# Kernel optimization log

Hardware: AMD Instinct MI355X
Metric: run time of the kernel (lower is better)

The kernel has to match this reference:

```python
import jax, jax.numpy as jnp
import numpy as np

N, IN_RAW, H, E, UNROLLS = 1024, 10, 96, 16384, 2

def _p(key, shape):
    return jax.random.normal(key, shape, dtype=jnp.float32) * 0.05

def setup_inputs() -> dict:
    key = jax.random.key(0)
    ks = jax.random.split(key, 24)
    x = jax.random.normal(ks[0], (N, IN_RAW), dtype=jnp.float32)
    edge_index = jax.random.randint(ks[1], (2, E), 0, N, dtype=jnp.int64)
    adj = jax.random.randint(ks[2], (N, N), 0, 2, dtype=jnp.int32)
    return {
        'x': x, 'edge_index': edge_index, 'adj': adj,
        # init_layer
        'W_init': _p(ks[3], (H, IN_RAW - 1)), 'b_init': _p(ks[4], (H,)),
        # GatedGraphConv (num_layers=1): weight [H,H], GRUCell params
        'W_ggc': _p(ks[5], (H, H)),
        'W_ih': _p(ks[6], (3 * H, H)), 'W_hh': _p(ks[7], (3 * H, H)),
        'b_ih': _p(ks[8], (3 * H,)), 'b_hh': _p(ks[9], (3 * H,)),
        # edge_attention: Linear(2H->H), Linear(H->1)
        'Wa1': _p(ks[10], (H, 2 * H)), 'ba1': _p(ks[11], (H,)),
        'Wa2': _p(ks[12], (1, H)), 'ba2': _p(ks[13], (1,)),
        # out MLP
        'Wo1': _p(ks[14], (H, H)), 'bo1': _p(ks[15], (H,)),
        'Wo2': _p(ks[16], (H, H)), 'bo2': _p(ks[17], (H,)),
        # heads
        'Wp1': _p(ks[18], (1, H)), 'bp1': _p(ks[19], (1,)),
        'Wp2': _p(ks[20], (1, H)), 'bp2': _p(ks[21], (1,)),
    }

def _leaky(v):
    return jnp.where(v >= 0, v, 0.01 * v)  # LeakyReLU default slope

def _ggnn_forward(x, edge_index, adj,
                  W_init, b_init, W_ggc, W_ih, W_hh, b_ih, b_hh,
                  Wa1, ba1, Wa2, ba2, Wo1, bo1, Wo2, bo2,
                  Wp1, bp1, Wp2, bp2):
    src, tgt = edge_index[0], edge_index[1]
    x = x[:, :-1]                                   # data.x[:, :-1]
    x = _leaky(x @ W_init.T + b_init)               # [N,H]
    adj_mask = (adj == 1)
    for _ in range(UNROLLS):
        # GatedGraphConv, 1 layer, aggr='mean'
        m = x @ W_ggc                               # [N,H]
        s = jax.ops.segment_sum(m[src], tgt, num_segments=N)
        cnt = jax.ops.segment_sum(jnp.ones((E,), x.dtype), tgt, num_segments=N)
        agg = s / jnp.maximum(cnt, 1.0)[:, None]    # mean, 0 for isolated nodes
        # GRUCell(agg, x)
        gi = agg @ W_ih.T + b_ih
        gh = x @ W_hh.T + b_hh
        ir, iz, inn = jnp.split(gi, 3, axis=1)
        hr, hz, hn = jnp.split(gh, 3, axis=1)
        r = jax.nn.sigmoid(ir + hr)
        z = jax.nn.sigmoid(iz + hz)
        n = jnp.tanh(inn + r * hn)
        x = (1.0 - z) * n + z * x
        # edge attention: concat(x_i, x_j) -> Linear(2H->H) decomposed into
        # two [H,H] halves so the NxNx2H concat tensor is never materialized.
        hi = x @ Wa1[:, :H].T                       # acts on t1 (row i)
        hj = x @ Wa1[:, H:].T                       # acts on t2 (row j)
        h = jax.nn.sigmoid(hi[:, None, :] + hj[None, :, :] + ba1)  # [N,N,H]
        coeffs = jax.nn.sigmoid(h @ Wa2[0] + ba2[0])               # [N,N]
        coeffs = jnp.where(adj_mask, coeffs, 0.0)
        x = coeffs @ x
    x = _leaky(x @ Wo1.T + bo1)
    x = _leaky(x @ Wo2.T + bo2)
    out1 = jax.nn.sigmoid(x @ Wp1.T + bp1)
    out2 = jax.nn.sigmoid(x @ Wp2.T + bp2)
    return out1, out2

def reference(x, edge_index, adj,
              W_init, b_init, W_ggc, W_ih, W_hh, b_ih, b_hh,
              Wa1, ba1, Wa2, ba2, Wo1, bo1, Wo2, bo2,
              Wp1, bp1, Wp2, bp2):
    return _ggnn_forward(x, edge_index, adj,
                         W_init, b_init, W_ggc, W_ih, W_hh, b_ih, b_hh,
                         Wa1, ba1, Wa2, ba2, Wo1, bo1, Wo2, bo2,
                         Wp1, bp1, Wp2, bp2)
```

## Files before the change

### kernel.cpp

```cpp
#include <hip/hip_runtime.h>

#define Nn 1024
#define Hh 96
#define Ee 16384
#define IN_K 9
#define IN_STRIDE 10
#define NH (Nn * Hh)
#define XS 128
#define SLOTS 64

__device__ __forceinline__ float sigf(float v) {
    return __builtin_amdgcn_rcpf(1.0f + __expf(-v));
}
__device__ __forceinline__ float tanhfast(float v) {
    float e = __expf(2.0f * v);
    return (e - 1.0f) * __builtin_amdgcn_rcpf(e + 1.0f);
}
__device__ __forceinline__ float leakyf(float v) {
    return v >= 0.0f ? v : 0.01f * v;
}

__global__ __launch_bounds__(256) void setup_kernel(
    const float* __restrict__ W_hh, const float* __restrict__ Wa1,
    const float* __restrict__ Wo1, const float* __restrict__ Wo2,
    const float* __restrict__ W_ggc, const float* __restrict__ W_ih,
    const float* __restrict__ x_in, const float* __restrict__ W_init,
    const float* __restrict__ b_init,
    float* __restrict__ Wt_hh, float* __restrict__ Wt_a1i,
    float* __restrict__ Wt_a1j, float* __restrict__ Wt_o1,
    float* __restrict__ Wt_o2, float* __restrict__ Wf,
    int* __restrict__ deg, float* __restrict__ xA)
{
    int gt = blockIdx.x * 256 + threadIdx.x;
    if (gt < Nn) deg[gt] = 0;
    if (gt < 64512) {
        int idx = gt;
        if (idx < 27648) {
            int k = idx / 288, c = idx % 288;
            Wt_hh[idx] = W_hh[c * 96 + k];
        } else if ((idx -= 27648) < 9216) {
            int k = idx / 96, h = idx % 96;
            Wt_a1i[idx] = Wa1[h * 192 + k];
        } else if ((idx -= 9216) < 9216) {
            int k = idx / 96, h = idx % 96;
            Wt_a1j[idx] = Wa1[h * 192 + 96 + k];
        } else if ((idx -= 9216) < 9216) {
            int k = idx / 96, j = idx % 96;
            Wt_o1[idx] = Wo1[j * 96 + k];
        } else {
            idx -= 9216;
            int k = idx / 96, j = idx % 96;
            Wt_o2[idx] = Wo2[j * 96 + k];
        }
    }
    if (gt < 27648) {
        int k = gt / 288, c = gt % 288;
        const float* g = W_ggc + k * 96;
        const float* w = W_ih + c * 96;
        float acc = 0.0f;
        for (int j = 0; j < 96; ++j) acc += g[j] * w[j];
        Wf[gt] = acc;
    }
    if (gt < NH) {
        int n = gt / Hh, j = gt - n * Hh;
        const float* xr = x_in + n * IN_STRIDE;
        const float* wr = W_init + j * IN_K;
        float acc = b_init[j];
#pragma unroll
        for (int k = 0; k < IN_K; ++k) acc += xr[k] * wr[k];
        xA[n * XS + j] = leakyf(acc);
    }
}

__global__ __launch_bounds__(256) void edges_kernel(
    const int* __restrict__ ei, int* __restrict__ deg, int* __restrict__ bucket)
{
    int e = blockIdx.x * 256 + threadIdx.x;
    if (e >= Ee) return;
    int src = ei[e];
    int tgt = ei[Ee + e];
    int slot = atomicAdd(&deg[tgt], 1);
    if (slot < SLOTS) bucket[tgt * SLOTS + slot] = src;
}

__global__ __launch_bounds__(384) void gru_kernel(
    const float* __restrict__ xA, const int* __restrict__ deg,
    const int* __restrict__ bucket,
    const float* __restrict__ Wf, const float* __restrict__ Wt_hh,
    const float* __restrict__ b_ih, const float* __restrict__ b_hh,
    const float* __restrict__ Wt_a1i, const float* __restrict__ Wt_a1j,
    const float* __restrict__ ba1,
    float* __restrict__ xB, float* __restrict__ Ei, float* __restrict__ EjT)
{
    __shared__ float Pp[2][2][Hh];
    __shared__ float Pm[2][Hh];
    __shared__ float Xr[2][Hh];
    __shared__ float Xo[2][Hh];
    __shared__ float red6[2][2][Hh][6];
    __shared__ float redp[2][2][Hh][2];
    int tid = threadIdx.x;
    int half = tid / 192;
    int loc = tid - half * 192;
    int r = loc / Hh, h = loc - r * Hh;
    int n = blockIdx.x * 2 + r;
    {
        int d = deg[n];
        int dc = d < SLOTS ? d : SLOTS;
        const int* bk = bucket + n * SLOTS;
        float acc = 0.0f;
        for (int s = half; s < dc; s += 2)
            acc += xA[bk[s] * XS + h];
        Pp[half][r][h] = acc;
        if (half == 0) Xr[r][h] = xA[n * XS + h];
    }
    __syncthreads();
    if (half == 0) {
        float inv = __builtin_amdgcn_rcpf(fmaxf((float)deg[n], 1.0f));
        Pm[r][h] = (Pp[0][r][h] + Pp[1][r][h]) * inv;
    }
    __syncthreads();
    {
        const float* Pr = Pm[r];
        const float* xr = Xr[r];
        const float* pf = Wf + h;
        const float* ph = Wt_hh + h;
        float gir = 0.f, giz = 0.f, gin = 0.f;
        float ghr = 0.f, ghz = 0.f, ghn = 0.f;
        int k0 = half * 48;
#pragma unroll 4
        for (int k = k0; k < k0 + 48; ++k) {
            float a = Pr[k];
            float xv = xr[k];
            int o = k * 288;
            gir += a * pf[o];
            giz += a * pf[o + 96];
            gin += a * pf[o + 192];
            ghr += xv * ph[o];
            ghz += xv * ph[o + 96];
            ghn += xv * ph[o + 192];
        }
        red6[half][r][h][0] = gir;
        red6[half][r][h][1] = giz;
        red6[half][r][h][2] = gin;
        red6[half][r][h][3] = ghr;
        red6[half][r][h][4] = ghz;
        red6[half][r][h][5] = ghn;
    }
    __syncthreads();
    if (half == 0) {
        float gir = b_ih[h] + red6[0][r][h][0] + red6[1][r][h][0];
        float giz = b_ih[Hh + h] + red6[0][r][h][1] + red6[1][r][h][1];
        float gin = b_ih[2 * Hh + h] + red6[0][r][h][2] + red6[1][r][h][2];
        float ghr = b_hh[h] + red6[0][r][h][3] + red6[1][r][h][3];
        float ghz = b_hh[Hh + h] + red6[0][r][h][4] + red6[1][r][h][4];
        float ghn = b_hh[2 * Hh + h] + red6[0][r][h][5] + red6[1][r][h][5];
        float rr = sigf(gir + ghr);
        float z = sigf(giz + ghz);
        float nn2 = tanhfast(gin + rr * ghn);
        float xo = (1.0f - z) * nn2 + z * Xr[r][h];
        xB[n * XS + h] = xo;
        Xo[r][h] = xo;
    }
    __syncthreads();
    {
        const float* row = Xo[r];
        const float* wi = Wt_a1i + h;
        const float* wj = Wt_a1j + h;
        float a = 0.0f, bb = 0.0f;
        int k0 = half * 48;
#pragma unroll 4
        for (int k = k0; k < k0 + 48; ++k) {
            float xv = row[k];
            a += xv * wi[k * 96];
            bb += xv * wj[k * 96];
        }
        redp[half][r][h][0] = a;
        redp[half][r][h][1] = bb;
    }
    __syncthreads();
    if (half == 0) {
        float a = redp[0][r][h][0] + redp[1][r][h][0];
        float bb = redp[0][r][h][1] + redp[1][r][h][1];
        Ei[n * Hh + h] = __expf(-(a + ba1[h]));
        EjT[h * Nn + n] = __expf(-bb);
    }
}

template <bool HEAD>
__global__ __launch_bounds__(512) void attn_kernel(
    const float* __restrict__ Ei, const float* __restrict__ EjT,
    const float* __restrict__ Wa2, const float* __restrict__ ba2,
    const int* __restrict__ adj, const float* __restrict__ xB,
    float* __restrict__ xA,
    const float* __restrict__ Wt_o1, const float* __restrict__ bo1,
    const float* __restrict__ Wt_o2, const float* __restrict__ bo2,
    const float* __restrict__ Wp1, const float* __restrict__ bp1,
    const float* __restrict__ Wp2, const float* __restrict__ bp2,
    float* __restrict__ out)
{
    __shared__ __align__(16) float wa2[Hh];
    __shared__ __align__(16) float eis[2][Hh];
    __shared__ __align__(16) float C[2][Nn];
    __shared__ float red[4][2][Hh];
    __shared__ float xout[2][Hh];
    __shared__ float t1[2][Hh];
    __shared__ float t2[2][Hh];
    int tid = threadIdx.x;
    int i0 = blockIdx.x * 2;
    if (tid < Hh) wa2[tid] = Wa2[tid];
    if (tid < 2 * Hh) {
        int r = tid / Hh, h = tid - r * Hh;
        eis[r][h] = Ei[(i0 + r) * Hh + h];
    }
    __syncthreads();
    {
        int row = tid >> 8;
        int jj = (tid & 255) * 4;
        int4 mk = *(const int4*)(adj + (i0 + row) * Nn + jj);
        float s0 = 0.f, s1 = 0.f, s2 = 0.f, s3 = 0.f;
        const float* er = eis[row];
#pragma unroll 4
        for (int k = 0; k < Hh; ++k) {
            float4 e4 = *(const float4*)(EjT + k * Nn + jj);
            float eik = er[k];
            float wk = wa2[k];
            s0 += __builtin_amdgcn_rcpf(fmaf(eik, e4.x, 1.0f)) * wk;
            s1 += __builtin_amdgcn_rcpf(fmaf(eik, e4.y, 1.0f)) * wk;
            s2 += __builtin_amdgcn_rcpf(fmaf(eik, e4.z, 1.0f)) * wk;
            s3 += __builtin_amdgcn_rcpf(fmaf(eik, e4.w, 1.0f)) * wk;
        }
        float b2 = ba2[0];
        float4 c;
        c.x = (mk.x == 1) ? sigf(s0 + b2) : 0.0f;
        c.y = (mk.y == 1) ? sigf(s1 + b2) : 0.0f;
        c.z = (mk.z == 1) ? sigf(s2 + b2) : 0.0f;
        c.w = (mk.w == 1) ? sigf(s3 + b2) : 0.0f;
        *(float4*)(&C[row][jj]) = c;
    }
    __syncthreads();
    {
        int q = tid >> 7;
        int h = tid & 127;
        if (h < Hh) {
            const float* xc = xB + h;
            int jb = q * 256;
            const float* c0 = &C[0][jb];
            const float* c1 = &C[1][jb];
            float acc0 = 0.f, acc1 = 0.f;
#pragma unroll 4
            for (int j = 0; j < 256; ++j) {
                float xv = xc[(jb + j) * XS];
                acc0 += c0[j] * xv;
                acc1 += c1[j] * xv;
            }
            red[q][0][h] = acc0;
            red[q][1][h] = acc1;
        }
        __syncthreads();
        if (q == 0 && h < Hh) {
#pragma unroll
            for (int r = 0; r < 2; ++r) {
                float v = red[0][r][h] + red[1][r][h] + red[2][r][h] + red[3][r][h];
                if (HEAD) xout[r][h] = v;
                else      xA[(i0 + r) * XS + h] = v;
            }
        }
    }
    if (HEAD) {
        __syncthreads();
        if (tid < 2 * Hh) {
            int r = tid / Hh, h = tid - r * Hh;
            const float* w = Wt_o1 + h;
            float acc = bo1[h];
            for (int k = 0; k < Hh; ++k) acc += xout[r][k] * w[k * 96];
            t1[r][h] = leakyf(acc);
        }
        __syncthreads();
        if (tid < 2 * Hh) {
            int r = tid / Hh, h = tid - r * Hh;
            const float* w = Wt_o2 + h;
            float acc = bo2[h];
            for (int k = 0; k < Hh; ++k) acc += t1[r][k] * w[k * 96];
            t2[r][h] = leakyf(acc);
        }
        __syncthreads();
        if (tid < 4) {
            int r = tid >> 1, which = tid & 1;
            const float* wp = which ? Wp2 : Wp1;
            float acc = 0.f;
            for (int k = 0; k < Hh; ++k) acc += t2[r][k] * wp[k];
            float b = which ? bp2[0] : bp1[0];
            out[which * Nn + i0 + r] = sigf(acc + b);
        }
    }
}

extern "C" void kernel_launch(void* const* d_in, const int* in_sizes, int n_in,
                              void* d_out, int out_size, void* d_ws, size_t ws_size,
                              hipStream_t stream)
{
    const float* x_in   = (const float*)d_in[0];
    const int*   ei     = (const int*)d_in[1];
    const int*   adj    = (const int*)d_in[2];
    const float* W_init = (const float*)d_in[3];
    const float* b_init = (const float*)d_in[4];
    const float* W_ggc  = (const float*)d_in[5];
    const float* W_ih   = (const float*)d_in[6];
    const float* W_hh   = (const float*)d_in[7];
    const float* b_ih   = (const float*)d_in[8];
    const float* b_hh   = (const float*)d_in[9];
    const float* Wa1    = (const float*)d_in[10];
    const float* ba1    = (const float*)d_in[11];
    const float* Wa2    = (const float*)d_in[12];
    const float* ba2    = (const float*)d_in[13];
    const float* Wo1    = (const float*)d_in[14];
    const float* bo1    = (const float*)d_in[15];
    const float* Wo2    = (const float*)d_in[16];
    const float* bo2    = (const float*)d_in[17];
    const float* Wp1    = (const float*)d_in[18];
    const float* bp1    = (const float*)d_in[19];
    const float* Wp2    = (const float*)d_in[20];
    const float* bp2    = (const float*)d_in[21];
    float* out = (float*)d_out;

    float* ws     = (float*)d_ws;
    float* xA     = ws;
    float* xB     = xA + Nn * XS;
    float* Ei     = xB + Nn * XS;
    float* EjT    = Ei + NH;
    float* Wt_hh  = EjT + NH;
    float* Wf     = Wt_hh + 27648;
    float* Wt_a1i = Wf + 27648;
    float* Wt_a1j = Wt_a1i + 9216;
    float* Wt_o1  = Wt_a1j + 9216;
    float* Wt_o2  = Wt_o1 + 9216;
    int*   deg    = (int*)(Wt_o2 + 9216);
    int*   bucket = deg + Nn;

    setup_kernel<<<(NH + 255) / 256, 256, 0, stream>>>(
        W_hh, Wa1, Wo1, Wo2, W_ggc, W_ih, x_in, W_init, b_init,
        Wt_hh, Wt_a1i, Wt_a1j, Wt_o1, Wt_o2, Wf, deg, xA);
    edges_kernel<<<(Ee + 255) / 256, 256, 0, stream>>>(ei, deg, bucket);

    gru_kernel<<<Nn / 2, 384, 0, stream>>>(
        xA, deg, bucket, Wf, Wt_hh, b_ih, b_hh, Wt_a1i, Wt_a1j, ba1,
        xB, Ei, EjT);
    attn_kernel<false><<<Nn / 2, 512, 0, stream>>>(
        Ei, EjT, Wa2, ba2, adj, xB, xA,
        nullptr, nullptr, nullptr, nullptr, nullptr, nullptr, nullptr, nullptr,
        nullptr);
    gru_kernel<<<Nn / 2, 384, 0, stream>>>(
        xA, deg, bucket, Wf, Wt_hh, b_ih, b_hh, Wt_a1i, Wt_a1j, ba1,
        xB, Ei, EjT);
    attn_kernel<true><<<Nn / 2, 512, 0, stream>>>(
        Ei, EjT, Wa2, ba2, adj, xB, xA,
        Wt_o1, bo1, Wt_o2, bo2, Wp1, bp1, Wp2, bp2, out);
}
```

Before: 211.3 us.

## Retile attention to 4 rows x half-columns with atomic accumulation and separate head kernel

The attention kernel now gives each block 4 target rows and half of the j columns instead of 2 rows and all columns. Each EjT load is reused across 4 rows, and each xB load in the coeffs@x product is reused across 4 accumulators. Partial sums from the two column halves are combined with atomicAdd into an output buffer that the previous GRU pass zeroes, using ping-pong buffers. The MLP head moves into its own kernel, which adds a launch plus atomic traffic and makes the summation order nondeterministic.

```diff
diff --git a/kernel.cpp b/kernel.cpp
--- a/kernel.cpp
+++ b/kernel.cpp
@@ -90,7 +90,8 @@
     const float* __restrict__ b_ih, const float* __restrict__ b_hh,
     const float* __restrict__ Wt_a1i, const float* __restrict__ Wt_a1j,
     const float* __restrict__ ba1,
-    float* __restrict__ xB, float* __restrict__ Ei, float* __restrict__ EjT)
+    float* __restrict__ xB, float* __restrict__ Ei, float* __restrict__ EjT,
+    float* __restrict__ xZero)
 {
     __shared__ float Pp[2][2][Hh];
     __shared__ float Pm[2][Hh];
@@ -112,6 +113,7 @@
             acc += xA[bk[s] * XS + h];
         Pp[half][r][h] = acc;
         if (half == 0) Xr[r][h] = xA[n * XS + h];
+        else           xZero[n * XS + h] = 0.0f;
     }
     __syncthreads();
     if (half == 0) {
@@ -186,112 +188,120 @@
     }
 }
 
-template <bool HEAD>
 __global__ __launch_bounds__(512) void attn_kernel(
     const float* __restrict__ Ei, const float* __restrict__ EjT,
     const float* __restrict__ Wa2, const float* __restrict__ ba2,
     const int* __restrict__ adj, const float* __restrict__ xB,
-    float* __restrict__ xA,
+    float* __restrict__ xOut)
+{
+    __shared__ __align__(16) float wa2[Hh];
+    __shared__ __align__(16) float eis[4][Hh];
+    __shared__ __align__(16) float C[4][512];
+    __shared__ float red[4][4][Hh];
+    int tid = threadIdx.x;
+    int ig = blockIdx.x >> 1;
+    int jh = blockIdx.x & 1;
+    int i0 = ig * 4;
+    int jbase = jh * 512;
+    if (tid < Hh) wa2[tid] = Wa2[tid];
+    if (tid < 4 * Hh) {
+        int r = tid / Hh, h = tid - r * Hh;
+        eis[r][h] = Ei[(i0 + r) * Hh + h];
+    }
+    __syncthreads();
+    {
+        int j = jbase + tid;
+        int m0 = adj[(i0 + 0) * Nn + j];
+        int m1 = adj[(i0 + 1) * Nn + j];
+        int m2 = adj[(i0 + 2) * Nn + j];
+        int m3 = adj[(i0 + 3) * Nn + j];
+        float s0 = 0.f, s1 = 0.f, s2 = 0.f, s3 = 0.f;
+#pragma unroll 4
+        for (int k = 0; k < Hh; ++k) {
+            float e = EjT[k * Nn + j];
+            float wk = wa2[k];
+            s0 += __builtin_amdgcn_rcpf(fmaf(eis[0][k], e, 1.0f)) * wk;
+            s1 += __builtin_amdgcn_rcpf(fmaf(eis[1][k], e, 1.0f)) * wk;
+            s2 += __builtin_amdgcn_rcpf(fmaf(eis[2][k], e, 1.0f)) * wk;
+            s3 += __builtin_amdgcn_rcpf(fmaf(eis[3][k], e, 1.0f)) * wk;
+        }
+        float b2 = ba2[0];
+        C[0][tid] = (m0 == 1) ? sigf(s0 + b2) : 0.0f;
+        C[1][tid] = (m1 == 1) ? sigf(s1 + b2) : 0.0f;
+        C[2][tid] = (m2 == 1) ? sigf(s2 + b2) : 0.0f;
+        C[3][tid] = (m3 == 1) ? sigf(s3 + b2) : 0.0f;
+    }
+    __syncthreads();
+    {
+        int q = tid >> 7;
+        int h = tid & 127;
+        if (h < Hh) {
+            int jq = q * 128;
+            const float* xc = xB + (jbase + jq) * XS + h;
+            const float* c0 = &C[0][jq];
+            const float* c1 = &C[1][jq];
+            const float* c2 = &C[2][jq];
+            const float* c3 = &C[3][jq];
+            float a0 = 0.f, a1 = 0.f, a2 = 0.f, a3 = 0.f;
+#pragma unroll 4
+            for (int j = 0; j < 128; ++j) {
+                float xv = xc[j * XS];
+                a0 += c0[j] * xv;
+                a1 += c1[j] * xv;
+                a2 += c2[j] * xv;
+                a3 += c3[j] * xv;
+            }
+            red[q][0][h] = a0;
+            red[q][1][h] = a1;
+            red[q][2][h] = a2;
+            red[q][3][h] = a3;
+        }
+        __syncthreads();
+        if (h < Hh) {
+            float v = red[0][q][h] + red[1][q][h] + red[2][q][h] + red[3][q][h];
+            atomicAdd(&xOut[(i0 + q) * XS + h], v);
+        }
+    }
+}
+
+__global__ __launch_bounds__(384) void head_kernel(
+    const float* __restrict__ xA,
     const float* __restrict__ Wt_o1, const float* __restrict__ bo1,
     const float* __restrict__ Wt_o2, const float* __restrict__ bo2,
     const float* __restrict__ Wp1, const float* __restrict__ bp1,
     const float* __restrict__ Wp2, const float* __restrict__ bp2,
     float* __restrict__ out)
 {
-    __shared__ __align__(16) float wa2[Hh];
-    __shared__ __align__(16) float eis[2][Hh];
-    __shared__ __align__(16) float C[2][Nn];
-    __shared__ float red[4][2][Hh];
-    __shared__ float xout[2][Hh];
-    __shared__ float t1[2][Hh];
-    __shared__ float t2[2][Hh];
+    __shared__ float xr[4][Hh];
+    __shared__ float t1[4][Hh];
+    __shared__ float t2[4][Hh];
     int tid = threadIdx.x;
-    int i0 = blockIdx.x * 2;
-    if (tid < Hh) wa2[tid] = Wa2[tid];
-    if (tid < 2 * Hh) {
-        int r = tid / Hh, h = tid - r * Hh;
-        eis[r][h] = Ei[(i0 + r) * Hh + h];
-    }
-    __syncthreads();
-    {
-        int row = tid >> 8;
-        int jj = (tid & 255) * 4;
-        int4 mk = *(const int4*)(adj + (i0 + row) * Nn + jj);
-        float s0 = 0.f, s1 = 0.f, s2 = 0.f, s3 = 0.f;
-        const float* er = eis[row];
-#pragma unroll 4
-        for (int k = 0; k < Hh; ++k) {
-            float4 e4 = *(const float4*)(EjT + k * Nn + jj);
-            float eik = er[k];
-            float wk = wa2[k];
-            s0 += __builtin_amdgcn_rcpf(fmaf(eik, e4.x, 1.0f)) * wk;
-            s1 += __builtin_amdgcn_rcpf(fmaf(eik, e4.y, 1.0f)) * wk;
-            s2 += __builtin_amdgcn_rcpf(fmaf(eik, e4.z, 1.0f)) * wk;
-            s3 += __builtin_amdgcn_rcpf(fmaf(eik, e4.w, 1.0f)) * wk;
-        }
-        float b2 = ba2[0];
-        float4 c;
-        c.x = (mk.x == 1) ? sigf(s0 + b2) : 0.0f;
-        c.y = (mk.y == 1) ? sigf(s1 + b2) : 0.0f;
-        c.z = (mk.z == 1) ? sigf(s2 + b2) : 0.0f;
-        c.w = (mk.w == 1) ? sigf(s3 + b2) : 0.0f;
-        *(float4*)(&C[row][jj]) = c;
-    }
-    __syncthreads();
-    {
-        int q = tid >> 7;
-        int h = tid & 127;
-        if (h < Hh) {
-            const float* xc = xB + h;
-            int jb = q * 256;
-            const float* c0 = &C[0][jb];
-            const float* c1 = &C[1][jb];
-            float acc0 = 0.f, acc1 = 0.f;
-#pragma unroll 4
-            for (int j = 0; j < 256; ++j) {
-                float xv = xc[(jb + j) * XS];
-                acc0 += c0[j] * xv;
-                acc1 += c1[j] * xv;
-            }
-            red[q][0][h] = acc0;
-            red[q][1][h] = acc1;
-        }
-        __syncthreads();
-        if (q == 0 && h < Hh) {
-#pragma unroll
-            for (int r = 0; r < 2; ++r) {
-                float v = red[0][r][h] + red[1][r][h] + red[2][r][h] + red[3][r][h];
-                if (HEAD) xout[r][h] = v;
-                else      xA[(i0 + r) * XS + h] = v;
-            }
-        }
-    }
-    if (HEAD) {
-        __syncthreads();
-        if (tid < 2 * Hh) {
-            int r = tid / Hh, h = tid - r * Hh;
-            const float* w = Wt_o1 + h;
-            float acc = bo1[h];
-            for (int k = 0; k < Hh; ++k) acc += xout[r][k] * w[k * 96];
-            t1[r][h] = leakyf(acc);
-        }
-        __syncthreads();
-        if (tid < 2 * Hh) {
-            int r = tid / Hh, h = tid - r * Hh;
-            const float* w = Wt_o2 + h;
-            float acc = bo2[h];
-            for (int k = 0; k < Hh; ++k) acc += t1[r][k] * w[k * 96];
-            t2[r][h] = leakyf(acc);
-        }
-        __syncthreads();
-        if (tid < 4) {
-            int r = tid >> 1, which = tid & 1;
-            const float* wp = which ? Wp2 : Wp1;
-            float acc = 0.f;
-            for (int k = 0; k < Hh; ++k) acc += t2[r][k] * wp[k];
-            float b = which ? bp2[0] : bp1[0];
-            out[which * Nn + i0 + r] = sigf(acc + b);
-        }
+    int r = tid / Hh, h = tid - r * Hh;
+    int n = blockIdx.x * 4 + r;
+    xr[r][h] = xA[n * XS + h];
+    __syncthreads();
+    {
+        const float* w = Wt_o1 + h;
+        float acc = bo1[h];
+        for (int k = 0; k < Hh; ++k) acc += xr[r][k] * w[k * 96];
+        t1[r][h] = leakyf(acc);
+    }
+    __syncthreads();
+    {
+        const float* w = Wt_o2 + h;
+        float acc = bo2[h];
+        for (int k = 0; k < Hh; ++k) acc += t1[r][k] * w[k * 96];
+        t2[r][h] = leakyf(acc);
+    }
+    __syncthreads();
+    if (h == 0) {
+        float s1 = 0.f;
+        for (int k = 0; k < Hh; ++k) s1 += t2[r][k] * Wp1[k];
+        out[n] = sigf(s1 + bp1[0]);
+    } else if (h == 1) {
+        float s2 = 0.f;
+        for (int k = 0; k < Hh; ++k) s2 += t2[r][k] * Wp2[k];
+        out[Nn + n] = sigf(s2 + bp2[0]);
     }
 }
 
@@ -326,7 +336,8 @@
     float* ws     = (float*)d_ws;
     float* xA     = ws;
     float* xB     = xA + Nn * XS;
-    float* Ei     = xB + Nn * XS;
+    float* xC     = xB + Nn * XS;
+    float* Ei     = xC + Nn * XS;
     float* EjT    = Ei + NH;
     float* Wt_hh  = EjT + NH;
     float* Wf     = Wt_hh + 27648;
@@ -344,15 +355,15 @@
 
     gru_kernel<<<Nn / 2, 384, 0, stream>>>(
         xA, deg, bucket, Wf, Wt_hh, b_ih, b_hh, Wt_a1i, Wt_a1j, ba1,
-        xB, Ei, EjT);
-    attn_kernel<false><<<Nn / 2, 512, 0, stream>>>(
-        Ei, EjT, Wa2, ba2, adj, xB, xA,
-        nullptr, nullptr, nullptr, nullptr, nullptr, nullptr, nullptr, nullptr,
-        nullptr);
+        xB, Ei, EjT, xC);
+    attn_kernel<<<Nn / 2, 512, 0, stream>>>(
+        Ei, EjT, Wa2, ba2, adj, xB, xC);
     gru_kernel<<<Nn / 2, 384, 0, stream>>>(
-        xA, deg, bucket, Wf, Wt_hh, b_ih, b_hh, Wt_a1i, Wt_a1j, ba1,
-        xB, Ei, EjT);
-    attn_kernel<true><<<Nn / 2, 512, 0, stream>>>(
-        Ei, EjT, Wa2, ba2, adj, xB, xA,
-        Wt_o1, bo1, Wt_o2, bo2, Wp1, bp1, Wp2, bp2, out);
-}
+        xC, deg, bucket, Wf, Wt_hh, b_ih, b_hh, Wt_a1i, Wt_a1j, ba1,
+        xB, Ei, EjT, xA);
+    attn_kernel<<<Nn / 2, 512, 0, stream>>>(
+        Ei, EjT, Wa2, ba2, adj, xB, xA);
+
+    head_kernel<<<Nn / 4, 384, 0, stream>>>(
+        xA, Wt_o1, bo1, Wt_o2, bo2, Wp1, bp1, Wp2, bp2, out);
+}
```

New measurement: 197.3 us. 6.6% less time.
